# Performance work log

Measured on AMD Instinct MI355X. Metric: run time of the kernel, lower is better.

The kernel has to match this reference:

```python
import jax, jax.numpy as jnp
import numpy as np

N = 100000
E = 1600000
IN_C, HID, OUT_C = 40, 64, 3


def _glorot(key, shape):
    fan_in, fan_out = shape[1], shape[0]
    lim = float(np.sqrt(6.0 / (fan_in + fan_out)))
    return jax.random.uniform(key, shape, jnp.float32, -lim, lim)


def setup_inputs() -> dict:
    key = jax.random.key(0)
    ks = jax.random.split(key, 12)
    x = jax.random.normal(ks[0], (N, IN_C), dtype=jnp.float32)
    edge_index = jax.random.randint(ks[1], (2, E), 0, N, dtype=jnp.int64)
    # Layer dims: 40->64, 64->128, 128->3. PyG SAGEConv: lin_l (neighbor, with bias), lin_r (root, no bias).
    params = {
        'W1l': _glorot(ks[2], (HID, IN_C)), 'b1': jnp.zeros((HID,), jnp.float32), 'W1r': _glorot(ks[3], (HID, IN_C)),
        'W2l': _glorot(ks[4], (2 * HID, HID)), 'b2': jnp.zeros((2 * HID,), jnp.float32), 'W2r': _glorot(ks[5], (2 * HID, HID)),
        'W4l': _glorot(ks[6], (OUT_C, 2 * HID)), 'b4': jnp.zeros((OUT_C,), jnp.float32), 'W4r': _glorot(ks[7], (OUT_C, 2 * HID)),
    }
    return {'x': x, 'edge_index': edge_index, **params}


def _sage_conv(x, src, dst, deg_inv, Wl, bl, Wr):
    # mean-aggregate neighbor messages x[src] at dst, then lin_l(agg) + lin_r(x) + b
    msgs = x[src]                                            # [E, F]
    agg = jax.ops.segment_sum(msgs, dst, num_segments=N)     # [N, F]
    mean = agg * deg_inv[:, None]
    return mean @ Wl.T + bl + x @ Wr.T


def reference(x, edge_index, W1l, b1, W1r, W2l, b2, W2r, W4l, b4, W4r):
    src, dst = edge_index[0], edge_index[1]
    deg = jax.ops.segment_sum(jnp.ones((E,), x.dtype), dst, num_segments=N)
    deg_inv = jnp.where(deg > 0, 1.0 / jnp.maximum(deg, 1.0), 0.0)
    h = jax.nn.relu(_sage_conv(x, src, dst, deg_inv, W1l, b1, W1r))
    h = jax.nn.relu(_sage_conv(h, src, dst, deg_inv, W2l, b2, W2r))
    h = _sage_conv(h, src, dst, deg_inv, W4l, b4, W4r)
    return h
```

## Files before the change

### kernel.cpp

```cpp
#include <hip/hip_runtime.h>
#include <hip/hip_bf16.h>


static constexpr int NN = 100000;
static constexpr int EE = 1600000;
static constexpr int NRANGE = 256;
static constexpr int RSIZE = (NN + NRANGE - 1) / NRANGE;
static constexpr int RPAD = 512;
static constexpr int NBUCKET = 8 * NRANGE;
static constexpr int CAP = 1024;
static constexpr int BCHUNK = 2048;
static constexpr int BUCKET_BLOCKS = (EE + BCHUNK - 1) / BCHUNK;
static constexpr int CVT_BLOCKS = (NN * 8 + 255) / 256;
static constexpr int NCHUNK16 = NN / 16;
static constexpr int EIDX = 512;

static constexpr int W1OFF = 0;
static constexpr int W2OFF = 4 * 4 * 64 * 8;
static constexpr int W4OFF = W2OFF + 8 * 4 * 64 * 8;
static constexpr int WPACK_SHORTS = W4OFF + 4 * 64 * 8;
static constexpr int PACK_ITEMS = 4 * 4 * 64 + 8 * 4 * 64 + 4 * 64;
static constexpr int PACK_BLOCKS = (PACK_ITEMS + 255) / 256;

typedef __attribute__((ext_vector_type(8))) short short8;
typedef __attribute__((ext_vector_type(4))) float f32x4;

__device__ __forceinline__ float bf2f(unsigned short u) {
    union { unsigned int i; float f; } c; c.i = ((unsigned int)u) << 16; return c.f;
}
__device__ __forceinline__ unsigned short f2bf(float f) {
    union { float f; unsigned int i; } c; c.f = f;
    unsigned int x = c.i;
    return (unsigned short)((x + 0x7fffu + ((x >> 16) & 1u)) >> 16);
}

__global__ __launch_bounds__(256) void k_bucket_cvt(const int* __restrict__ src, const int* __restrict__ dst,
                                                    int* __restrict__ pcur, unsigned int* __restrict__ pairs,
                                                    const float* __restrict__ x, unsigned short* __restrict__ xb,
                                                    const float* __restrict__ W1l, const float* __restrict__ W1r,
                                                    const float* __restrict__ W2l, const float* __restrict__ W2r,
                                                    const float* __restrict__ W4l, const float* __restrict__ W4r,
                                                    unsigned short* __restrict__ wpack) {
    __shared__ int cnt[NRANGE];
    __shared__ int base[NRANGE];
    const int tid = threadIdx.x;
    if (blockIdx.x >= BUCKET_BLOCKS + CVT_BLOCKS) {
        int idx = (blockIdx.x - BUCKET_BLOCKS - CVT_BLOCKS) * 256 + tid;
        if (idx < PACK_ITEMS) {
            short8 v;
            if (idx < 1024) {
                int l = idx & 63, ks = (idx >> 6) & 3, t = idx >> 8;
                int o = t * 16 + (l & 15);
                int kbase = ks * 32 + (l >> 4) * 8;
#pragma unroll
                for (int j = 0; j < 8; ++j) {
                    int k = kbase + j; float w;
                    if (k < 64) w = (k < 40) ? W1l[o * 40 + k] : 0.f;
                    else { int k2 = k - 64; w = (k2 < 40) ? W1r[o * 40 + k2] : 0.f; }
                    v[j] = (short)f2bf(w);
                }
                *(short8*)&wpack[W1OFF + idx * 8] = v;
            } else if (idx < 3072) {
                int i2 = idx - 1024;
                int l = i2 & 63, ks = (i2 >> 6) & 3, t = i2 >> 8;
                int o = t * 16 + (l & 15);
                int kbase = ks * 32 + (l >> 4) * 8;
#pragma unroll
                for (int j = 0; j < 8; ++j) {
                    int k = kbase + j;
                    float w = (k < 64) ? W2l[o * 64 + k] : W2r[o * 64 + (k - 64)];
                    v[j] = (short)f2bf(w);
                }
                *(short8*)&wpack[W2OFF + i2 * 8] = v;
            } else {
                int i4 = idx - 3072;
                int l = i4 & 63, ks = i4 >> 6;
                int o = l & 15;
                int kbase = ks * 32 + (l >> 4) * 8;
#pragma unroll
                for (int j = 0; j < 8; ++j) {
                    int k = kbase + j;
                    float w = 0.f;
                    if (o < 3) w = W4l[o * 128 + k];
                    else if (o >= 4 && o < 7) w = W4r[(o - 4) * 128 + k];
                    v[j] = (short)f2bf(w);
                }
                *(short8*)&wpack[W4OFF + i4 * 8] = v;
            }
        }
        return;
    }
    if (blockIdx.x >= BUCKET_BLOCKS) {
        int i = (blockIdx.x - BUCKET_BLOCKS) * 256 + tid;
        if (i < NN * 8) {
            int node = i >> 3, c = i & 7;
            short8 v = {0, 0, 0, 0, 0, 0, 0, 0};
            if (c < 5) {
                const float4* p = (const float4*)(x + (size_t)node * 40 + c * 8);
                float4 a = p[0], b = p[1];
                v[0] = (short)f2bf(a.x); v[1] = (short)f2bf(a.y); v[2] = (short)f2bf(a.z); v[3] = (short)f2bf(a.w);
                v[4] = (short)f2bf(b.x); v[5] = (short)f2bf(b.y); v[6] = (short)f2bf(b.z); v[7] = (short)f2bf(b.w);
            }
            *(short8*)(xb + (size_t)i * 8) = v;
        }
        return;
    }
    const int part = blockIdx.x & 7;
    const int e0 = blockIdx.x * BCHUNK;
    cnt[tid] = 0;
    __syncthreads();
    int r_[8], lp_[8];
    unsigned int p_[8];
#pragma unroll
    for (int j = 0; j < 8; ++j) {
        int e = e0 + j * 256 + tid;
        r_[j] = -1;
        if (e < EE) {
            int d = dst[e];
            int s = src[e];
            int r = d / RSIZE;
            r_[j] = r;
            p_[j] = (unsigned int)s | ((unsigned int)(d - r * RSIZE) << 17);
            lp_[j] = atomicAdd(&cnt[r], 1);
        }
    }
    __syncthreads();
    {
        int c = cnt[tid];
        base[tid] = (c > 0) ? atomicAdd(&pcur[(part << 8) | tid], c) : 0;
    }
    __syncthreads();
#pragma unroll
    for (int j = 0; j < 8; ++j) {
        if (r_[j] >= 0) {
            int pos = base[r_[j]] + lp_[j];
            if (pos < CAP) pairs[(size_t)((part << 8) | r_[j]) * CAP + pos] = p_[j];
        }
    }
}

__global__ __launch_bounds__(1024) void k_build(const unsigned int* __restrict__ pairs,
                                                const int* __restrict__ pcur,
                                                int* __restrict__ row_start, float* __restrict__ deg_inv,
                                                int* __restrict__ csr_src) {
    __shared__ int ldeg[RPAD];
    __shared__ int lrs[RPAD];
    __shared__ int rtot[NRANGE];
    const int tid = threadIdx.x;
    const int r = blockIdx.x;
    const int lo = r * RSIZE;
    const int nloc = (lo + RSIZE <= NN) ? RSIZE : (NN - lo);
    for (int t = tid; t < RPAD; t += 1024) ldeg[t] = 0;
    __syncthreads();
    for (int p = 0; p < 8; ++p) {
        int b = (p << 8) | r;
        int len = pcur[b]; if (len > CAP) len = CAP;
        const unsigned int* bp = pairs + (size_t)b * CAP;
        for (int i = tid; i < len; i += 1024)
            atomicAdd(&ldeg[bp[i] >> 17], 1);
    }
    if (tid < NRANGE) {
        int s = 0;
#pragma unroll
        for (int p = 0; p < 8; ++p) {
            int c = pcur[(p << 8) | tid];
            s += (c > CAP) ? CAP : c;
        }
        rtot[tid] = s;
    }
    __syncthreads();
    for (int d = 1; d < NRANGE; d <<= 1) {
        int t = (tid < NRANGE && tid >= d) ? rtot[tid - d] : 0;
        __syncthreads();
        if (tid < NRANGE) rtot[tid] += t;
        __syncthreads();
    }
    const int rbase = (r == 0) ? 0 : rtot[r - 1];
    if (tid < RPAD) lrs[tid] = ldeg[tid];
    __syncthreads();
    for (int d = 1; d < RPAD; d <<= 1) {
        int t = (tid < RPAD && tid >= d) ? lrs[tid - d] : 0;
        __syncthreads();
        if (tid < RPAD) lrs[tid] += t;
        __syncthreads();
    }
    int excl = 0, dg = 0;
    if (tid < RPAD) { dg = ldeg[tid]; excl = lrs[tid] - dg; }
    if (tid < nloc) {
        row_start[lo + tid] = rbase + excl;
        deg_inv[lo + tid] = (dg > 0) ? 1.0f / (float)dg : 0.0f;
    }
    if (r == 0 && tid == 0) row_start[NN] = EE;
    __syncthreads();
    if (tid < RPAD) { lrs[tid] = excl; ldeg[tid] = 0; }
    __syncthreads();
    for (int p = 0; p < 8; ++p) {
        int b = (p << 8) | r;
        int len = pcur[b]; if (len > CAP) len = CAP;
        const unsigned int* bp = pairs + (size_t)b * CAP;
        for (int i = tid; i < len; i += 1024) {
            unsigned int pk = bp[i];
            int dloc = pk >> 17;
            int lp = atomicAdd(&ldeg[dloc], 1);
            csr_src[rbase + lrs[dloc] + lp] = (int)(pk & 0x1FFFFu);
        }
    }
}

template<int Fout, bool RELU, bool ZR, int WOFF>
__global__ __launch_bounds__(128, 8) void k_fused(const unsigned short* __restrict__ xin,
                                                  const int* __restrict__ row_start,
                                                  const int* __restrict__ csr_src,
                                                  const float* __restrict__ deg_inv,
                                                  const unsigned short* __restrict__ wpack,
                                                  const float* __restrict__ bias,
                                                  unsigned short* __restrict__ out,
                                                  float* __restrict__ z,
                                                  float* __restrict__ rr_) {
    constexpr int KS = 4;
    constexpr int TILES = Fout / 16;
    constexpr int TPW = TILES / 2;
    constexpr int SMEAN = 0;
    constexpr int SROOT = 16 * 72;
    constexpr int SH2 = 2 * 16 * 72;
    constexpr int SHM = 2 * 16 * 72 + (ZR ? 16 * 136 : 0);
    __shared__ short shm[SHM];
    __shared__ int lidx[EIDX];
    const int tid = threadIdx.x;
    const int lane = tid & 63;
    const int wv = tid >> 6;
    const int nbase = blockIdx.x * 16;

    float bias_t[TPW];
#pragma unroll
    for (int tt = 0; tt < TPW; ++tt) bias_t[tt] = bias[(wv * TPW + tt) * 16 + (lane & 15)];

    const int rs_blk = row_start[nbase];
    const int re_blk = row_start[nbase + 16];
    const int nedge = re_blk - rs_blk;
    for (int i = tid; i < nedge && i < EIDX; i += 128) lidx[i] = csr_src[rs_blk + i];
    __syncthreads();

    const int node8 = tid >> 3;
    const int c = tid & 7;

    {
        const int node = nbase + node8;
        float acc[8] = {0, 0, 0, 0, 0, 0, 0, 0};
        const unsigned short* xq = xin + c * 8;
        const int rs = row_start[node], re = row_start[node + 1];
        int k = rs;
        for (; k + 4 <= re; k += 4) {
            short8 v[4];
#pragma unroll
            for (int j = 0; j < 4; ++j) {
                int off = k + j - rs_blk;
                int s = (off < EIDX) ? lidx[off] : csr_src[k + j];
                v[j] = *(const short8*)(xq + (size_t)s * 64);
            }
#pragma unroll
            for (int j = 0; j < 4; ++j)
#pragma unroll
                for (int t = 0; t < 8; ++t) acc[t] += bf2f((unsigned short)v[j][t]);
        }
        if (k < re) {
            short8 v[4];
#pragma unroll
            for (int j = 0; j < 4; ++j) {
                int kk = (k + j < re) ? (k + j) : (re - 1);
                int off = kk - rs_blk;
                int s = (off < EIDX) ? lidx[off] : csr_src[kk];
                v[j] = *(const short8*)(xq + (size_t)s * 64);
            }
#pragma unroll
            for (int j = 0; j < 4; ++j) {
                float m = (k + j < re) ? 1.f : 0.f;
#pragma unroll
                for (int t = 0; t < 8; ++t) acc[t] += m * bf2f((unsigned short)v[j][t]);
            }
        }
        float di = deg_inv[node];
        short8 mv;
#pragma unroll
        for (int t = 0; t < 8; ++t) mv[t] = (short)f2bf(acc[t] * di);
        short8 rv = *(const short8*)(xin + (size_t)node * 64 + c * 8);
        *(short8*)&shm[SMEAN + node8 * 72 + c * 8] = mv;
        *(short8*)&shm[SROOT + node8 * 72 + c * 8] = rv;
    }
    __syncthreads();
    short8 af[KS];
#pragma unroll
    for (int ks = 0; ks < KS; ++ks) {
        const int base = (ks < 2) ? SMEAN : SROOT;
        const int g = (ks & 1) * 4 + (lane >> 4);
        af[ks] = *(const short8*)&shm[base + (lane & 15) * 72 + g * 8];
    }
    f32x4 acc2[TPW];
#pragma unroll
    for (int tt = 0; tt < TPW; ++tt) acc2[tt] = (f32x4){0.f, 0.f, 0.f, 0.f};
#pragma unroll
    for (int tt = 0; tt < TPW; ++tt) {
        short8 bt[KS];
#pragma unroll
        for (int ks = 0; ks < KS; ++ks)
            bt[ks] = *(const short8*)&wpack[WOFF + (((wv * TPW + tt) * KS + ks) * 64 + lane) * 8];
#pragma unroll
        for (int ks = 0; ks < KS; ++ks)
            acc2[tt] = __builtin_amdgcn_mfma_f32_16x16x32_bf16(af[ks], bt[ks], acc2[tt], 0, 0, 0);
    }
    if constexpr (!ZR) {
        const int nrow = nbase + (lane >> 4) * 4;
#pragma unroll
        for (int tt = 0; tt < TPW; ++tt) {
            int col = (wv * TPW + tt) * 16 + (lane & 15);
#pragma unroll
            for (int q = 0; q < 4; ++q) {
                float v = acc2[tt][q] + bias_t[tt];
                if (RELU) v = fmaxf(v, 0.f);
                out[(size_t)(nrow + q) * Fout + col] = f2bf(v);
            }
        }
    } else {
        const int row0 = (lane >> 4) * 4;
#pragma unroll
        for (int tt = 0; tt < TPW; ++tt) {
            int col = (wv * TPW + tt) * 16 + (lane & 15);
#pragma unroll
            for (int q = 0; q < 4; ++q) {
                float v = acc2[tt][q] + bias_t[tt];
                if (RELU) v = fmaxf(v, 0.f);
                shm[SH2 + (row0 + q) * 136 + col] = (short)f2bf(v);
            }
        }
        __syncthreads();
        if (wv == 0) {
            short8 b4r[4];
#pragma unroll
            for (int ks = 0; ks < 4; ++ks)
                b4r[ks] = *(const short8*)&wpack[W4OFF + (ks * 64 + lane) * 8];
            const int row = lane & 15;
            f32x4 az = (f32x4){0.f, 0.f, 0.f, 0.f};
#pragma unroll
            for (int ks = 0; ks < 4; ++ks) {
                short8 a4 = *(const short8*)&shm[SH2 + row * 136 + (ks * 4 + (lane >> 4)) * 8];
                az = __builtin_amdgcn_mfma_f32_16x16x32_bf16(a4, b4r[ks], az, 0, 0, 0);
            }
            const int col = lane & 15;
            const int nr = nbase + (lane >> 4) * 4;
            if (col < 3) {
#pragma unroll
                for (int q = 0; q < 4; ++q) z[(size_t)(nr + q) * 4 + col] = az[q];
            } else if (col >= 4 && col < 7) {
#pragma unroll
                for (int q = 0; q < 4; ++q) rr_[(size_t)(nr + q) * 4 + col - 4] = az[q];
            }
        }
    }
}

__global__ __launch_bounds__(256) void k_final(const float* __restrict__ z, const float* __restrict__ r,
                                               const float* __restrict__ b4,
                                               const int* __restrict__ row_start, const int* __restrict__ csr_src,
                                               const float* __restrict__ deg_inv, float* __restrict__ out) {
    int n = blockIdx.x * 256 + threadIdx.x;
    if (n >= NN) return;
    const int rs = row_start[n], re = row_start[n + 1];
    float a0 = 0, a1 = 0, a2 = 0, b0 = 0, b1 = 0, b2 = 0;
    const float4* z4 = (const float4*)z;
    int k = rs;
    for (; k + 8 <= re; k += 8) {
        int e[8];
#pragma unroll
        for (int j = 0; j < 8; ++j) e[j] = csr_src[k + j];
        float4 v[8];
#pragma unroll
        for (int j = 0; j < 8; ++j) v[j] = z4[e[j]];
#pragma unroll
        for (int j = 0; j < 8; j += 2) {
            a0 += v[j].x; a1 += v[j].y; a2 += v[j].z;
            b0 += v[j + 1].x; b1 += v[j + 1].y; b2 += v[j + 1].z;
        }
    }
    if (k < re) {
        int e[8];
#pragma unroll
        for (int j = 0; j < 8; ++j) e[j] = csr_src[(k + j < re) ? (k + j) : (re - 1)];
        float4 v[8];
#pragma unroll
        for (int j = 0; j < 8; ++j) v[j] = z4[e[j]];
#pragma unroll
        for (int j = 0; j < 8; ++j) {
            float m = (k + j < re) ? 1.f : 0.f;
            a0 += m * v[j].x; a1 += m * v[j].y; a2 += m * v[j].z;
        }
    }
    float di = deg_inv[n];
    float4 rn = *(const float4*)&r[4 * (size_t)n];
    out[(size_t)n * 3 + 0] = (a0 + b0) * di + rn.x + b4[0];
    out[(size_t)n * 3 + 1] = (a1 + b1) * di + rn.y + b4[1];
    out[(size_t)n * 3 + 2] = (a2 + b2) * di + rn.z + b4[2];
}

extern "C" void kernel_launch(void* const* d_in, const int* in_sizes, int n_in,
                              void* d_out, int out_size, void* d_ws, size_t ws_size,
                              hipStream_t stream) {
    const float* x   = (const float*)d_in[0];
    const int*   ei  = (const int*)d_in[1];
    const float* W1l = (const float*)d_in[2];
    const float* b1  = (const float*)d_in[3];
    const float* W1r = (const float*)d_in[4];
    const float* W2l = (const float*)d_in[5];
    const float* b2  = (const float*)d_in[6];
    const float* W2r = (const float*)d_in[7];
    const float* W4l = (const float*)d_in[8];
    const float* b4  = (const float*)d_in[9];
    const float* W4r = (const float*)d_in[10];
    float* out = (float*)d_out;

    char* ws = (char*)d_ws;
    size_t off = 0;
    auto alloc = [&](size_t bytes) -> void* {
        void* p = ws + off;
        off = (off + bytes + 255) & ~(size_t)255;
        return p;
    };
    int*   row_start = (int*)alloc(((size_t)NN + 1) * 4);
    int*   csr_src   = (int*)alloc((size_t)EE * 4);
    float* deg_inv   = (float*)alloc((size_t)NN * 4);
    int*   pcur      = (int*)alloc((size_t)NBUCKET * 4);
    unsigned short* xb    = (unsigned short*)alloc((size_t)NN * 64 * 2);
    unsigned short* h1    = (unsigned short*)alloc((size_t)NN * 64 * 2);
    unsigned short* wpack = (unsigned short*)alloc((size_t)WPACK_SHORTS * 2);
    float* zbuf = (float*)alloc((size_t)NN * 4 * 4);
    float* rbuf = (float*)alloc((size_t)NN * 4 * 4);
    unsigned int* pairs = (unsigned int*)alloc((size_t)NBUCKET * CAP * 4);

    const int* e_src = ei;
    const int* e_dst = ei + EE;

    hipMemsetAsync(pcur, 0, (size_t)NBUCKET * 4, stream);

    k_bucket_cvt<<<BUCKET_BLOCKS + CVT_BLOCKS + PACK_BLOCKS, 256, 0, stream>>>(
        e_src, e_dst, pcur, pairs, x, xb, W1l, W1r, W2l, W2r, W4l, W4r, wpack);
    k_build<<<NRANGE, 1024, 0, stream>>>(pairs, pcur, row_start, deg_inv, csr_src);

    k_fused<64, true, false, W1OFF><<<NCHUNK16, 128, 0, stream>>>(
        xb, row_start, csr_src, deg_inv, wpack, b1, h1, nullptr, nullptr);
    k_fused<128, true, true, W2OFF><<<NCHUNK16, 128, 0, stream>>>(
        h1, row_start, csr_src, deg_inv, wpack, b2, nullptr, zbuf, rbuf);
    k_final<<<(NN + 255) / 256, 256, 0, stream>>>(zbuf, rbuf, b4, row_start, csr_src, deg_inv, out);
}
```

Measured before the change: 192.5 us.

## Balance edge gather across node groups with LDS atomic accumulation

Replaces the per-node gather loop, where each 8-thread group handled one destination node, with an edge-balanced split: the block's edge range is divided evenly among the 16 groups, and partial sums are flushed into a shared float accumulator with LDS atomics whenever a group crosses a node boundary. Degree inverse is recomputed from row offsets in shared memory instead of being loaded. The aim is to remove load imbalance from variable in-degree within a block. In exchange it adds LDS atomics, extra shared memory per block and an extra barrier, which may lower occupancy.

```diff
diff --git a/kernel.cpp b/kernel.cpp
--- a/kernel.cpp
+++ b/kernel.cpp
@@ -211,7 +211,6 @@
 __global__ __launch_bounds__(128, 8) void k_fused(const unsigned short* __restrict__ xin,
                                                   const int* __restrict__ row_start,
                                                   const int* __restrict__ csr_src,
-                                                  const float* __restrict__ deg_inv,
                                                   const unsigned short* __restrict__ wpack,
                                                   const float* __restrict__ bias,
                                                   unsigned short* __restrict__ out,
@@ -225,7 +224,9 @@
     constexpr int SH2 = 2 * 16 * 72;
     constexpr int SHM = 2 * 16 * 72 + (ZR ? 16 * 136 : 0);
     __shared__ short shm[SHM];
+    __shared__ float facc[16][64];
     __shared__ int lidx[EIDX];
+    __shared__ int rsl[17];
     const int tid = threadIdx.x;
     const int lane = tid & 63;
     const int wv = tid >> 6;
@@ -236,56 +237,67 @@
     for (int tt = 0; tt < TPW; ++tt) bias_t[tt] = bias[(wv * TPW + tt) * 16 + (lane & 15)];
 
     const int rs_blk = row_start[nbase];
-    const int re_blk = row_start[nbase + 16];
-    const int nedge = re_blk - rs_blk;
+    if (tid < 17) rsl[tid] = row_start[nbase + tid] - rs_blk;
+    {
+        float4* fz = (float4*)facc;
+        fz[tid * 2] = (float4){0.f, 0.f, 0.f, 0.f};
+        fz[tid * 2 + 1] = (float4){0.f, 0.f, 0.f, 0.f};
+    }
+    const int nedge = row_start[nbase + 16] - rs_blk;
     for (int i = tid; i < nedge && i < EIDX; i += 128) lidx[i] = csr_src[rs_blk + i];
     __syncthreads();
 
-    const int node8 = tid >> 3;
+    const int w8 = tid >> 3;
     const int c = tid & 7;
 
     {
-        const int node = nbase + node8;
-        float acc[8] = {0, 0, 0, 0, 0, 0, 0, 0};
-        const unsigned short* xq = xin + c * 8;
-        const int rs = row_start[node], re = row_start[node + 1];
-        int k = rs;
-        for (; k + 4 <= re; k += 4) {
-            short8 v[4];
-#pragma unroll
-            for (int j = 0; j < 4; ++j) {
-                int off = k + j - rs_blk;
-                int s = (off < EIDX) ? lidx[off] : csr_src[k + j];
-                v[j] = *(const short8*)(xq + (size_t)s * 64);
-            }
-#pragma unroll
-            for (int j = 0; j < 4; ++j)
-#pragma unroll
-                for (int t = 0; t < 8; ++t) acc[t] += bf2f((unsigned short)v[j][t]);
-        }
-        if (k < re) {
-            short8 v[4];
-#pragma unroll
-            for (int j = 0; j < 4; ++j) {
-                int kk = (k + j < re) ? (k + j) : (re - 1);
-                int off = kk - rs_blk;
-                int s = (off < EIDX) ? lidx[off] : csr_src[kk];
-                v[j] = *(const short8*)(xq + (size_t)s * 64);
-            }
-#pragma unroll
-            for (int j = 0; j < 4; ++j) {
-                float m = (k + j < re) ? 1.f : 0.f;
-#pragma unroll
-                for (int t = 0; t < 8; ++t) acc[t] += m * bf2f((unsigned short)v[j][t]);
-            }
-        }
-        float di = deg_inv[node];
+        const int len = rsl[16];
+        const int g0 = (w8 * len) >> 4;
+        const int g1 = ((w8 + 1) * len) >> 4;
+        if (g0 < g1) {
+            const unsigned short* xq = xin + c * 8;
+            int node = 0;
+            while (rsl[node + 1] <= g0) ++node;
+            int cur_end = rsl[node + 1];
+            float acc[8] = {0, 0, 0, 0, 0, 0, 0, 0};
+            int g = g0;
+            while (g < g1) {
+                const int take = (g1 - g < 4) ? (g1 - g) : 4;
+                short8 v[4];
+#pragma unroll
+                for (int j = 0; j < 4; ++j) {
+                    int gi = (j < take) ? (g + j) : (g1 - 1);
+                    int s = (gi < EIDX) ? lidx[gi] : csr_src[rs_blk + gi];
+                    v[j] = *(const short8*)(xq + (size_t)s * 64);
+                }
+#pragma unroll
+                for (int j = 0; j < 4; ++j) {
+                    if (j < take) {
+                        while (g + j >= cur_end) {
+#pragma unroll
+                            for (int t = 0; t < 8; ++t) { atomicAdd(&facc[node][c * 8 + t], acc[t]); acc[t] = 0.f; }
+                            ++node; cur_end = rsl[node + 1];
+                        }
+#pragma unroll
+                        for (int t = 0; t < 8; ++t) acc[t] += bf2f((unsigned short)v[j][t]);
+                    }
+                }
+                g += 4;
+            }
+#pragma unroll
+            for (int t = 0; t < 8; ++t) atomicAdd(&facc[node][c * 8 + t], acc[t]);
+        }
+    }
+    __syncthreads();
+    {
+        const int dg = rsl[w8 + 1] - rsl[w8];
+        const float di = (dg > 0) ? 1.0f / (float)dg : 0.0f;
         short8 mv;
 #pragma unroll
-        for (int t = 0; t < 8; ++t) mv[t] = (short)f2bf(acc[t] * di);
-        short8 rv = *(const short8*)(xin + (size_t)node * 64 + c * 8);
-        *(short8*)&shm[SMEAN + node8 * 72 + c * 8] = mv;
-        *(short8*)&shm[SROOT + node8 * 72 + c * 8] = rv;
+        for (int t = 0; t < 8; ++t) mv[t] = (short)f2bf(facc[w8][c * 8 + t] * di);
+        short8 rv = *(const short8*)(xin + (size_t)(nbase + w8) * 64 + c * 8);
+        *(short8*)&shm[SMEAN + w8 * 72 + c * 8] = mv;
+        *(short8*)&shm[SROOT + w8 * 72 + c * 8] = rv;
     }
     __syncthreads();
     short8 af[KS];
@@ -445,8 +457,8 @@
     k_build<<<NRANGE, 1024, 0, stream>>>(pairs, pcur, row_start, deg_inv, csr_src);
 
     k_fused<64, true, false, W1OFF><<<NCHUNK16, 128, 0, stream>>>(
-        xb, row_start, csr_src, deg_inv, wpack, b1, h1, nullptr, nullptr);
+        xb, row_start, csr_src, wpack, b1, h1, nullptr, nullptr);
     k_fused<128, true, true, W2OFF><<<NCHUNK16, 128, 0, stream>>>(
-        h1, row_start, csr_src, deg_inv, wpack, b2, nullptr, zbuf, rbuf);
+        h1, row_start, csr_src, wpack, b2, nullptr, zbuf, rbuf);
     k_final<<<(NN + 255) / 256, 256, 0, stream>>>(zbuf, rbuf, b4, row_start, csr_src, deg_inv, out);
 }
```

After: 285.6 us. 48.4% more time.
